# Performance work log

Measured on AMD Instinct MI355X. Metric: run time of the kernel, lower is better.

## Reference

```python
import jax, jax.numpy as jnp
import numpy as np
from jax import lax

STRIDE = (2, 2)
PADDING = (1, 1)  # symmetric H/W padding, zeros mode, zero_point = 0.0


def setup_inputs() -> dict:
    key = jax.random.key(0)
    kx, kw = jax.random.split(key)
    x = jax.random.normal(kx, (8, 16, 1024, 1024), dtype=jnp.float32)
    # stored binary weight: values in {0,1}; decode maps 1 -> +1, else -> -1
    weight = jax.random.randint(kw, (16, 16, 3, 3), 0, 2).astype(jnp.float32)
    return {"x": x, "weight": weight}


def reference(x, weight):
    # decode: where(w == 1, w, -1)  (binarize to +/-1)
    decoded = jnp.where(weight == 1.0, weight, -jnp.ones_like(weight))
    # explicit zero padding (padding_mode='zeros', zero_point=0.0)
    xp = jnp.pad(x, ((0, 0), (0, 0), (PADDING[0], PADDING[0]), (PADDING[1], PADDING[1])))
    # conv2d, stride (2,2), no further padding, dilation 1, groups 1, no bias.
    # (Original emulates in float64; JAX default fp32 computes identical math
    # since weights are exactly +/-1 and accumulation fits fp32 here.)
    out = lax.conv_general_dilated(
        xp, decoded,
        window_strides=STRIDE,
        padding='VALID',
        dimension_numbers=('NCHW', 'OIHW', 'NCHW'),
    )
    return out.astype(jnp.float32)
```

## Files before the change

kernel.cpp:

```cpp
#include <hip/hip_runtime.h>


#define IN_H   1024
#define IN_W   1024
#define OUT_H  512
#define OUT_W  512
#define C_IN   16
#define C_OUT  16

#define TILE     16
#define TIN      33
#define TSTRIDE  33

__global__ void decode_weights(const float* __restrict__ w,
                               float* __restrict__ wdec) {
    int i = blockIdx.x * blockDim.x + threadIdx.x;
    if (i >= C_IN * 9 * C_OUT) return;
    int co  = i & 15;
    int t   = i >> 4;
    int tap = t % 9;
    int ci  = t / 9;
    float v = w[(co * C_IN + ci) * 9 + tap];
    wdec[i] = (v == 1.0f) ? 1.0f : -1.0f;
}

__global__ __launch_bounds__(256)
void binconv(const float* __restrict__ x,
             const float* __restrict__ wdec,
             float* __restrict__ out) {
    const int tx = threadIdx.x;
    const int ty = threadIdx.y;
    const int bx = blockIdx.x;
    const int by = blockIdx.y;
    const int n  = blockIdx.z;

    const int ow0 = bx * TILE;
    const int oh0 = by * TILE;
    const int gx0 = ow0 * 2 - 1;
    const int gy0 = oh0 * 2 - 1;

    __shared__ float tile[TIN * TSTRIDE];

    float acc[C_OUT];
#pragma unroll
    for (int co = 0; co < C_OUT; ++co) acc[co] = 0.0f;

    const int tid = ty * 16 + tx;
    const float* xn = x + (size_t)n * C_IN * IN_H * IN_W;

    for (int ci = 0; ci < C_IN; ++ci) {
        if (ci) __syncthreads();
        const float* xc = xn + (size_t)ci * IN_H * IN_W;

        for (int i = tid; i < TIN * TIN; i += 256) {
            int r = i / TIN;
            int c = i - r * TIN;
            int gy = gy0 + r;
            int gx = gx0 + c;
            float v = 0.0f;
            if ((unsigned)gy < (unsigned)IN_H && (unsigned)gx < (unsigned)IN_W)
                v = xc[gy * IN_W + gx];
            tile[r * TSTRIDE + c] = v;
        }
        __syncthreads();

        float xv[9];
#pragma unroll
        for (int ky = 0; ky < 3; ++ky)
#pragma unroll
            for (int kx = 0; kx < 3; ++kx)
                xv[ky * 3 + kx] = tile[(ty * 2 + ky) * TSTRIDE + tx * 2 + kx];

        const float* wc = wdec + ci * 9 * C_OUT;
#pragma unroll
        for (int t = 0; t < 9; ++t) {
            float xvt = xv[t];
#pragma unroll
            for (int co = 0; co < C_OUT; ++co)
                acc[co] = fmaf(wc[t * C_OUT + co], xvt, acc[co]);
        }
    }

    const int oh = oh0 + ty;
    const int ow = ow0 + tx;
    float* on = out + (size_t)n * C_OUT * OUT_H * OUT_W + oh * OUT_W + ow;
#pragma unroll
    for (int co = 0; co < C_OUT; ++co)
        on[(size_t)co * OUT_H * OUT_W] = acc[co];
}

extern "C" void kernel_launch(void* const* d_in, const int* in_sizes, int n_in,
                              void* d_out, int out_size, void* d_ws, size_t ws_size,
                              hipStream_t stream) {
    const float* x = (const float*)d_in[0];
    const float* w = (const float*)d_in[1];
    float* out = (float*)d_out;
    float* wdec = (float*)d_ws;

    decode_weights<<<dim3((C_IN * 9 * C_OUT + 255) / 256), dim3(256), 0, stream>>>(w, wdec);

    dim3 block(TILE, TILE, 1);
    dim3 grid(OUT_W / TILE, OUT_H / TILE, 8);
    binconv<<<grid, block, 0, stream>>>(x, wdec, out);
}
```

Baseline: 904.1 us.

## Replace LDS tiling with direct vectorized global loads and 64x4 blocks

Drops the shared-memory tile and its per-channel __syncthreads, so each thread reads its 3x3 window straight from global memory with one float2 load plus one scalar load per row, relying on cache for the overlap between neighbouring windows. The block shape changes to 64x4 so a wavefront covers a contiguous row of outputs, giving coalesced loads and stores, and launch bounds now request higher occupancy. This removes LDS traffic and barriers but puts more load on L1/L2 for the overlapping rows and columns.

New measurement: 739.4 us. -18.2%, faster.

```diff
diff --git a/kernel.cpp b/kernel.cpp
--- a/kernel.cpp
+++ b/kernel.cpp
@@ -7,10 +7,6 @@
 #define OUT_W  512
 #define C_IN   16
 #define C_OUT  16
-
-#define TILE     16
-#define TIN      33
-#define TSTRIDE  33
 
 __global__ void decode_weights(const float* __restrict__ w,
                                float* __restrict__ wdec) {
@@ -24,69 +20,60 @@
     wdec[i] = (v == 1.0f) ? 1.0f : -1.0f;
 }
 
-__global__ __launch_bounds__(256)
+__global__ __launch_bounds__(256, 8)
 void binconv(const float* __restrict__ x,
              const float* __restrict__ wdec,
              float* __restrict__ out) {
     const int tx = threadIdx.x;
     const int ty = threadIdx.y;
-    const int bx = blockIdx.x;
-    const int by = blockIdx.y;
+    const int ow = blockIdx.x * 64 + tx;
+    const int oh = blockIdx.y * 4 + ty;
     const int n  = blockIdx.z;
 
-    const int ow0 = bx * TILE;
-    const int oh0 = by * TILE;
-    const int gx0 = ow0 * 2 - 1;
-    const int gy0 = oh0 * 2 - 1;
+    const float* xn = x + (size_t)n * C_IN * IN_H * IN_W;
+    const int gx0 = 2 * ow - 1;
+    const int gy0 = 2 * oh - 1;
 
-    __shared__ float tile[TIN * TSTRIDE];
+    const bool row0_ok = (gy0 >= 0);
+    const bool colm_ok = (gx0 >= 0);
+    const int  gy0c    = row0_ok ? gy0 : 0;
+    const int  gxmc    = colm_ok ? gx0 : 0;
 
     float acc[C_OUT];
 #pragma unroll
     for (int co = 0; co < C_OUT; ++co) acc[co] = 0.0f;
 
-    const int tid = ty * 16 + tx;
-    const float* xn = x + (size_t)n * C_IN * IN_H * IN_W;
-
     for (int ci = 0; ci < C_IN; ++ci) {
-        if (ci) __syncthreads();
-        const float* xc = xn + (size_t)ci * IN_H * IN_W;
-
-        for (int i = tid; i < TIN * TIN; i += 256) {
-            int r = i / TIN;
-            int c = i - r * TIN;
-            int gy = gy0 + r;
-            int gx = gx0 + c;
-            float v = 0.0f;
-            if ((unsigned)gy < (unsigned)IN_H && (unsigned)gx < (unsigned)IN_W)
-                v = xc[gy * IN_W + gx];
-            tile[r * TSTRIDE + c] = v;
-        }
-        __syncthreads();
+        const float* xc = xn + (size_t)ci * (IN_H * IN_W);
 
         float xv[9];
 #pragma unroll
-        for (int ky = 0; ky < 3; ++ky)
-#pragma unroll
-            for (int kx = 0; kx < 3; ++kx)
-                xv[ky * 3 + kx] = tile[(ty * 2 + ky) * TSTRIDE + tx * 2 + kx];
+        for (int ky = 0; ky < 3; ++ky) {
+            const int gy = (ky == 0) ? gy0c : (gy0 + ky);
+            const float* xrow = xc + gy * IN_W;
+            float2 f2 = *(const float2*)&xrow[gx0 + 1];
+            float  sm = xrow[gxmc];
+            const bool rok = (ky == 0) ? row0_ok : true;
+            xv[ky * 3 + 0] = (rok && colm_ok) ? sm : 0.0f;
+            xv[ky * 3 + 1] = rok ? f2.x : 0.0f;
+            xv[ky * 3 + 2] = rok ? f2.y : 0.0f;
+        }
 
         const float* wc = wdec + ci * 9 * C_OUT;
 #pragma unroll
         for (int t = 0; t < 9; ++t) {
-            float xvt = xv[t];
+            const float xt = xv[t];
 #pragma unroll
             for (int co = 0; co < C_OUT; ++co)
-                acc[co] = fmaf(wc[t * C_OUT + co], xvt, acc[co]);
+                acc[co] = fmaf(wc[t * C_OUT + co], xt, acc[co]);
         }
     }
 
-    const int oh = oh0 + ty;
-    const int ow = ow0 + tx;
-    float* on = out + (size_t)n * C_OUT * OUT_H * OUT_W + oh * OUT_W + ow;
+    float* op = out + (size_t)n * C_OUT * OUT_H * OUT_W
+                    + (size_t)oh * OUT_W + ow;
 #pragma unroll
     for (int co = 0; co < C_OUT; ++co)
-        on[(size_t)co * OUT_H * OUT_W] = acc[co];
+        op[(size_t)co * OUT_H * OUT_W] = acc[co];
 }
 
 extern "C" void kernel_launch(void* const* d_in, const int* in_sizes, int n_in,
@@ -99,7 +86,7 @@
 
     decode_weights<<<dim3((C_IN * 9 * C_OUT + 255) / 256), dim3(256), 0, stream>>>(w, wdec);
 
-    dim3 block(TILE, TILE, 1);
-    dim3 grid(OUT_W / TILE, OUT_H / TILE, 8);
+    dim3 block(64, 4, 1);
+    dim3 grid(OUT_W / 64, OUT_H / 4, 8);
     binconv<<<grid, block, 0, stream>>>(x, wdec, out);
 }
```
